# Kernel optimization log

Measured on AMD Instinct MI355X. Metric: run time of the kernel, lower is better.

## Reference

```python
import jax, jax.numpy as jnp
import numpy as np

B, NQ, NK = 2, 1024, 1024
QD, KVD, OD = 1024, 1024, 1024
H, DH = 8, 64
INNER = H * DH  # 512
FF_INNER = 4 * OD


def _ln(x, w, b, eps=1e-5):
    m = jnp.mean(x, axis=-1, keepdims=True)
    v = jnp.mean((x - m) ** 2, axis=-1, keepdims=True)
    return (x - m) / jnp.sqrt(v + eps) * w + b


def _attn(q, k, v, h):
    # q:[b,nq,h*d] k,v:[b,nk,h*d] -> [b,nq,h*d]
    b, nq, _ = q.shape
    nk = k.shape[1]
    qh = q.reshape(b, nq, h, -1).transpose(0, 2, 1, 3)
    kh = k.reshape(b, nk, h, -1).transpose(0, 2, 1, 3)
    vh = v.reshape(b, nk, h, -1).transpose(0, 2, 1, 3)
    scale = qh.shape[-1] ** -0.5
    sim = jnp.einsum('bhid,bhjd->bhij', qh * scale, kh)
    a = jax.nn.softmax(sim, axis=-1)
    o = jnp.einsum('bhij,bhjd->bhid', a, vh)
    return o.transpose(0, 2, 1, 3).reshape(b, nq, -1)


def setup_inputs() -> dict:
    key = jax.random.key(0)
    ks = jax.random.split(key, 16)
    w = lambda k, shp: jax.random.normal(k, shp, dtype=jnp.float32) * 0.02
    return {
        'query_feats': jax.random.normal(ks[0], (B, NQ, QD), dtype=jnp.float32),
        'kv_feats_wt': jax.random.normal(ks[1], (B, NK, KVD), dtype=jnp.float32),
        'nq_w': jnp.ones((QD,), jnp.float32), 'nq_b': jnp.zeros((QD,), jnp.float32),
        'nkv_w': jnp.ones((KVD,), jnp.float32), 'nkv_b': jnp.zeros((KVD,), jnp.float32),
        'wq_cross': w(ks[2], (INNER, QD)),
        'wkv_cross': w(ks[3], (2 * INNER, KVD)),
        'wqkv_self': w(ks[4], (3 * INNER, QD)),
        'gn_w': jnp.ones((INNER,), jnp.float32), 'gn_b': jnp.zeros((INNER,), jnp.float32),
        'mha_in_w': w(ks[5], (3 * INNER, INNER)),
        'mha_out_w': w(ks[6], (INNER, INNER)),
        'mix_w': w(ks[7], (2, INNER)), 'mix_b': jnp.zeros((2,), jnp.float32),
        'w_out': w(ks[8], (OD, INNER)),
        'ff_ln_w': jnp.ones((OD,), jnp.float32), 'ff_ln_b': jnp.zeros((OD,), jnp.float32),
        'ff_fc1': w(ks[9], (FF_INNER, OD)),
        'ff_fc2': w(ks[10], (OD, FF_INNER)),
        'ff_gate': jnp.ones((1,), jnp.float32),
    }


def reference(query_feats, kv_feats_wt, nq_w, nq_b, nkv_w, nkv_b, wq_cross,
              wkv_cross, wqkv_self, gn_w, gn_b, mha_in_w, mha_out_w, mix_w,
              mix_b, w_out, ff_ln_w, ff_ln_b, ff_fc1, ff_fc2, ff_gate):
    # mode == 'full'
    kvn = _ln(kv_feats_wt, nkv_w, nkv_b)

    # wt self-attention branch
    qkv_wt = kvn @ wqkv_self.T
    q_wt, k_wt, v_wt = jnp.split(qkv_wt, 3, axis=-1)
    wt_out = _attn(q_wt, k_wt, v_wt, H) @ w_out.T

    qn = _ln(query_feats, nq_w, nq_b)

    # cross attention
    q_c = qn @ wq_cross.T
    k_c, v_c = jnp.split(kvn @ wkv_cross.T, 2, axis=-1)
    cross_out = _attn(q_c, k_c, v_c, H)

    # self attention on query
    q_s, k_s, v_s = jnp.split(qn @ wqkv_self.T, 3, axis=-1)
    self_out = _attn(q_s, k_s, v_s, H)

    # gating MHA (shared gate_norm)
    son = _ln(self_out, gn_w, gn_b)
    con = _ln(cross_out, gn_w, gn_b)
    wq_g, wk_g, wv_g = jnp.split(mha_in_w, 3, axis=0)
    gate_ctx = _attn(son @ wq_g.T, con @ wk_g.T, con @ wv_g.T, H) @ mha_out_w.T

    mix = jax.nn.softmax(gate_ctx @ mix_w.T + mix_b, axis=-1)
    mixed = mix[..., 0:1] * self_out + mix[..., 1:2] * cross_out
    delta = mixed @ w_out.T

    # FeedForward with gate
    y = _ln(delta, ff_ln_w, ff_ln_b)
    y = jax.nn.gelu(y @ ff_fc1.T, approximate=False) @ ff_fc2.T
    delta = delta + ff_gate * y

    return jnp.stack([delta, wt_out])  # [2, B, NQ, OD]
```

## Files before the change

### kernel.cpp

```cpp
#include <hip/hip_runtime.h>
#include <math.h>


#define M_ROWS 2048
#define SEQ    1024

typedef unsigned short u16;
typedef __attribute__((ext_vector_type(8))) short short8;
typedef __attribute__((ext_vector_type(4))) float f32x4;

__device__ inline u16 f2b(float f) {
    unsigned u = __builtin_bit_cast(unsigned, f);
    u += 0x7FFFu + ((u >> 16) & 1u);
    return (u16)(u >> 16);
}
__device__ inline float b2f(u16 h) {
    return __builtin_bit_cast(float, (unsigned)h << 16);
}

__device__ inline void gload16(const u16* g, u16* l) {
    __builtin_amdgcn_global_load_lds(
        (const __attribute__((address_space(1))) void*)g,
        (__attribute__((address_space(3))) void*)l, 16, 0, 0);
}

__device__ __forceinline__ int aswz(int prow, int chunk) {
    return prow * 32 + ((chunk ^ ((prow >> 1) & 3)) << 3);
}

struct CvtPack { const float* s[8]; u16* d[8]; };

__global__ __launch_bounds__(256)
void cvt8_kernel(CvtPack p)
{
    constexpr int pre[9] = {0, 1536, 2048, 3072, 3840, 4096, 4608, 8704, 12800};
    const int b = blockIdx.x;
    int seg = 0;
    #pragma unroll
    for (int i = 1; i < 8; ++i) seg += (b >= pre[i]);
    const int off = (b - pre[seg]) * 1024 + threadIdx.x * 4;
    const float4 v = *reinterpret_cast<const float4*>(p.s[seg] + off);
    ushort4 o;
    o.x = f2b(v.x); o.y = f2b(v.y); o.z = f2b(v.z); o.w = f2b(v.w);
    *reinterpret_cast<ushort4*>(p.d[seg] + off) = o;
}

__global__ __launch_bounds__(256)
void ln_dual(const float* __restrict__ x0, const float* __restrict__ w0,
             const float* __restrict__ b0, u16* __restrict__ out0,
             const float* __restrict__ x1, const float* __restrict__ w1,
             const float* __restrict__ b1, u16* __restrict__ out1, int D)
{
    const int r = blockIdx.x;
    const int sel = r >= M_ROWS;
    const size_t row = sel ? r - M_ROWS : r;
    const float* x = sel ? x1 : x0;
    const float* w = sel ? w1 : w0;
    const float* bias = sel ? b1 : b0;
    u16* out = sel ? out1 : out0;
    const float* xr = x + row * (size_t)D;
    const int c = threadIdx.x * 4;
    float4 v = make_float4(0.f, 0.f, 0.f, 0.f);
    if (c < D) v = *reinterpret_cast<const float4*>(&xr[c]);
    float sum = v.x + v.y + v.z + v.w;
    float sq  = v.x*v.x + v.y*v.y + v.z*v.z + v.w*v.w;
    #pragma unroll
    for (int off = 32; off > 0; off >>= 1) {
        sum += __shfl_down(sum, off);
        sq  += __shfl_down(sq,  off);
    }
    __shared__ float s1[4], s2[4];
    const int wid = threadIdx.x >> 6;
    if ((threadIdx.x & 63) == 0) { s1[wid] = sum; s2[wid] = sq; }
    __syncthreads();
    const float tsum = s1[0] + s1[1] + s1[2] + s1[3];
    const float tsq  = s2[0] + s2[1] + s2[2] + s2[3];
    const float mean = tsum / (float)D;
    const float var  = tsq / (float)D - mean * mean;
    const float rstd = rsqrtf(var + 1e-5f);
    if (c < D) {
        ushort4 o;
        o.x = f2b((v.x - mean) * rstd * w[c+0] + bias[c+0]);
        o.y = f2b((v.y - mean) * rstd * w[c+1] + bias[c+1]);
        o.z = f2b((v.z - mean) * rstd * w[c+2] + bias[c+2]);
        o.w = f2b((v.w - mean) * rstd * w[c+3] + bias[c+3]);
        *reinterpret_cast<ushort4*>(&out[row * (size_t)D + c]) = o;
    }
}

__global__ __launch_bounds__(256)
void ln_bf16(const float* __restrict__ x, const float* __restrict__ w,
             const float* __restrict__ bias, u16* __restrict__ out, int D)
{
    const size_t row = blockIdx.x;
    const float* xr = x + row * (size_t)D;
    const int c = threadIdx.x * 4;
    float4 v = make_float4(0.f, 0.f, 0.f, 0.f);
    if (c < D) v = *reinterpret_cast<const float4*>(&xr[c]);
    float sum = v.x + v.y + v.z + v.w;
    float sq  = v.x*v.x + v.y*v.y + v.z*v.z + v.w*v.w;
    #pragma unroll
    for (int off = 32; off > 0; off >>= 1) {
        sum += __shfl_down(sum, off);
        sq  += __shfl_down(sq,  off);
    }
    __shared__ float s1[4], s2[4];
    const int wid = threadIdx.x >> 6;
    if ((threadIdx.x & 63) == 0) { s1[wid] = sum; s2[wid] = sq; }
    __syncthreads();
    const float tsum = s1[0] + s1[1] + s1[2] + s1[3];
    const float tsq  = s2[0] + s2[1] + s2[2] + s2[3];
    const float mean = tsum / (float)D;
    const float var  = tsq / (float)D - mean * mean;
    const float rstd = rsqrtf(var + 1e-5f);
    if (c < D) {
        ushort4 o;
        o.x = f2b((v.x - mean) * rstd * w[c+0] + bias[c+0]);
        o.y = f2b((v.y - mean) * rstd * w[c+1] + bias[c+1]);
        o.z = f2b((v.z - mean) * rstd * w[c+2] + bias[c+2]);
        o.w = f2b((v.w - mean) * rstd * w[c+3] + bias[c+3]);
        *reinterpret_cast<ushort4*>(&out[row * (size_t)D + c]) = o;
    }
}

__device__ __forceinline__ void gemm64_core(
    const u16* __restrict__ A, const u16* __restrict__ W, void* __restrict__ C,
    int ob, int N, int K, int m0, int n0, u16* As, u16* Ws)
{
    constexpr int PF = 3, LPT = 2, RD = 4;
    const int tid  = threadIdx.x;
    const int lane = tid & 63;
    const int wave = tid >> 6;
    const int wr = wave >> 1, wc = wave & 1;

    const int srow = tid >> 2;
    const int scol = (((tid & 3) ^ ((srow >> 1) & 3))) * 8;
    const u16* Ag = A + (size_t)(m0 + srow) * K + scol;
    const u16* Wg = W + (size_t)(n0 + srow) * K + scol;

    const int fr = lane & 15;
    const int fq = lane >> 4;

    f32x4 acc[2][2] = {};

    auto stage = [&](int buf, int k0) {
        gload16(Ag + k0, &As[buf * 2048 + tid * 8]);
        gload16(Wg + k0, &Ws[buf * 2048 + tid * 8]);
    };
    auto compute = [&](int buf) {
        short8 a[2], b[2];
        #pragma unroll
        for (int m = 0; m < 2; ++m) {
            const int r = wr * 32 + m * 16 + fr;
            a[m] = *reinterpret_cast<const short8*>(&As[buf * 2048 + aswz(r, fq)]);
        }
        #pragma unroll
        for (int n = 0; n < 2; ++n) {
            const int r = wc * 32 + n * 16 + fr;
            b[n] = *reinterpret_cast<const short8*>(&Ws[buf * 2048 + aswz(r, fq)]);
        }
        #pragma unroll
        for (int m = 0; m < 2; ++m)
            #pragma unroll
            for (int n = 0; n < 2; ++n)
                acc[m][n] = __builtin_amdgcn_mfma_f32_16x16x32_bf16(
                    a[m], b[n], acc[m][n], 0, 0, 0);
    };

    const int nt = K / 32;
    #pragma unroll
    for (int i = 0; i < PF; ++i) stage(i, i * 32);

    int cbuf = 0, sbuf = PF;
    for (int t = 0; t <= nt - PF; ++t) {
        asm volatile("s_waitcnt vmcnt(%0)\n\ts_barrier"
                     :: "n"((PF - 1) * LPT) : "memory");
        if (t + PF < nt) {
            stage(sbuf, (t + PF) * 32);
            if (++sbuf == RD) sbuf = 0;
        }
        compute(cbuf);
        if (++cbuf == RD) cbuf = 0;
    }
    #pragma unroll
    for (int i = 1; i < PF; ++i) {
        asm volatile("s_waitcnt vmcnt(%0)\n\ts_barrier"
                     :: "n"((PF - 1 - i) * LPT) : "memory");
        compute(cbuf);
        if (++cbuf == RD) cbuf = 0;
    }

    #pragma unroll
    for (int m = 0; m < 2; ++m)
        #pragma unroll
        for (int j = 0; j < 4; ++j) {
            const size_t row = (size_t)(m0 + wr * 32 + m * 16 + fq * 4 + j);
            #pragma unroll
            for (int n = 0; n < 2; ++n) {
                const size_t idx = row * (size_t)N + (size_t)(n0 + wc * 32 + n * 16 + fr);
                if (ob) ((u16*)C)[idx]  = f2b(acc[m][n][j]);
                else    ((float*)C)[idx] = acc[m][n][j];
            }
        }
}

__device__ __forceinline__ void gemm128_core(
    const u16* __restrict__ A, const u16* __restrict__ W, u16* __restrict__ C,
    int N, int K, int m0, int n0, u16* As, u16* Ws)
{
    constexpr int PF = 3, LPT = 3, RD = 4;
    const int tid  = threadIdx.x;
    const int lane = tid & 63;
    const int wave = tid >> 6;
    const int wr = wave >> 1, wc = wave & 1;

    const int srow = tid >> 2;
    const int scol = (((tid & 3) ^ ((srow >> 1) & 3))) * 8;
    const u16* Ag = A + (size_t)(m0 + srow) * K + scol;
    const u16* Wg = W + (size_t)(n0 + srow) * K + scol;

    const int fr = lane & 15;
    const int fq = lane >> 4;

    f32x4 acc[4][2] = {};

    auto stage = [&](int buf, int k0) {
        gload16(Ag + k0,                  &As[buf * 4096 + tid * 8]);
        gload16(Ag + k0 + (size_t)64 * K, &As[buf * 4096 + tid * 8 + 2048]);
        gload16(Wg + k0,                  &Ws[buf * 2048 + tid * 8]);
    };
    auto compute = [&](int buf) {
        short8 a[4], b[2];
        #pragma unroll
        for (int m = 0; m < 4; ++m) {
            const int r = wr * 64 + m * 16 + fr;
            a[m] = *reinterpret_cast<const short8*>(&As[buf * 4096 + aswz(r, fq)]);
        }
        #pragma unroll
        for (int n = 0; n < 2; ++n) {
            const int r = wc * 32 + n * 16 + fr;
            b[n] = *reinterpret_cast<const short8*>(&Ws[buf * 2048 + aswz(r, fq)]);
        }
        #pragma unroll
        for (int m = 0; m < 4; ++m)
            #pragma unroll
            for (int n = 0; n < 2; ++n)
                acc[m][n] = __builtin_amdgcn_mfma_f32_16x16x32_bf16(
                    a[m], b[n], acc[m][n], 0, 0, 0);
    };

    const int nt = K / 32;
    #pragma unroll
    for (int i = 0; i < PF; ++i) stage(i, i * 32);

    int cbuf = 0, sbuf = PF;
    for (int t = 0; t <= nt - PF; ++t) {
        asm volatile("s_waitcnt vmcnt(%0)\n\ts_barrier"
                     :: "n"((PF - 1) * LPT) : "memory");
        if (t + PF < nt) {
            stage(sbuf, (t + PF) * 32);
            if (++sbuf == RD) sbuf = 0;
        }
        compute(cbuf);
        if (++cbuf == RD) cbuf = 0;
    }
    #pragma unroll
    for (int i = 1; i < PF; ++i) {
        asm volatile("s_waitcnt vmcnt(%0)\n\ts_barrier"
                     :: "n"((PF - 1 - i) * LPT) : "memory");
        compute(cbuf);
        if (++cbuf == RD) cbuf = 0;
    }

    #pragma unroll
    for (int m = 0; m < 4; ++m)
        #pragma unroll
        for (int j = 0; j < 4; ++j) {
            const size_t row = (size_t)(m0 + wr * 64 + m * 16 + fq * 4 + j);
            #pragma unroll
            for (int n = 0; n < 2; ++n)
                C[row * (size_t)N + (size_t)(n0 + wc * 32 + n * 16 + fr)] =
                    f2b(acc[m][n][j]);
        }
}

template<int BM, int BN, int EPI, int OB>
__global__ __launch_bounds__(256)
void gemm_mfma(const u16* __restrict__ A, const u16* __restrict__ W,
               void* __restrict__ Cv, int N, int K,
               const float* __restrict__ gatep, int kchunk)
{
    constexpr int MF  = BM / 32;
    constexpr int NF  = BN / 32;
    constexpr int LPT = BM / 64 + BN / 64;
    constexpr int PF  = 3;
    constexpr int RD  = 4;
    __shared__ __align__(16) u16 As[RD][BM * 32];
    __shared__ __align__(16) u16 Ws[RD][BN * 32];
    const int tid  = threadIdx.x;
    const int lane = tid & 63;
    const int wave = tid >> 6;
    const int wr = wave >> 1, wc = wave & 1;

    const int nwg = gridDim.x * gridDim.y;
    const int bid = blockIdx.y * gridDim.x + blockIdx.x;
    const int nid = (bid & 7) * (nwg >> 3) + (bid >> 3);
    const int by  = nid % gridDim.y;
    const int bx  = nid / gridDim.y;
    const int m0 = by * BM, n0 = bx * BN;
    const int kz = blockIdx.z * kchunk;

    const int srow = tid >> 2;
    const int scol = (((tid & 3) ^ ((srow >> 1) & 3))) * 8;
    const u16* Ag = A + (size_t)(m0 + srow) * K + scol + kz;
    const u16* Wg = W + (size_t)(n0 + srow) * K + scol + kz;

    const int fr = lane & 15;
    const int fq = lane >> 4;

    f32x4 acc[MF][NF] = {};

    auto stage = [&](int buf, int k0) {
        #pragma unroll
        for (int i = 0; i < BM / 64; ++i)
            gload16(Ag + k0 + (size_t)(i * 64) * K, &As[buf][tid * 8 + i * 2048]);
        #pragma unroll
        for (int i = 0; i < BN / 64; ++i)
            gload16(Wg + k0 + (size_t)(i * 64) * K, &Ws[buf][tid * 8 + i * 2048]);
    };
    auto compute = [&](int buf) {
        short8 a[MF], b[NF];
        #pragma unroll
        for (int m = 0; m < MF; ++m) {
            const int r = wr * (BM / 2) + m * 16 + fr;
            a[m] = *reinterpret_cast<const short8*>(&As[buf][aswz(r, fq)]);
        }
        #pragma unroll
        for (int n = 0; n < NF; ++n) {
            const int r = wc * (BN / 2) + n * 16 + fr;
            b[n] = *reinterpret_cast<const short8*>(&Ws[buf][aswz(r, fq)]);
        }
        #pragma unroll
        for (int m = 0; m < MF; ++m)
            #pragma unroll
            for (int n = 0; n < NF; ++n)
                acc[m][n] = __builtin_amdgcn_mfma_f32_16x16x32_bf16(
                    a[m], b[n], acc[m][n], 0, 0, 0);
    };

    const int nt = kchunk / 32;
    #pragma unroll
    for (int i = 0; i < PF; ++i) stage(i, i * 32);

    int cbuf = 0, sbuf = PF;
    for (int t = 0; t <= nt - PF; ++t) {
        asm volatile("s_waitcnt vmcnt(%0)\n\ts_barrier"
                     :: "n"((PF - 1) * LPT) : "memory");
        if (t + PF < nt) {
            stage(sbuf, (t + PF) * 32);
            if (++sbuf == RD) sbuf = 0;
        }
        compute(cbuf);
        if (++cbuf == RD) cbuf = 0;
    }
    #pragma unroll
    for (int i = 1; i < PF; ++i) {
        asm volatile("s_waitcnt vmcnt(%0)\n\ts_barrier"
                     :: "n"((PF - 1 - i) * LPT) : "memory");
        compute(cbuf);
        if (++cbuf == RD) cbuf = 0;
    }

    float* Cz = (float*)Cv + (size_t)blockIdx.z * M_ROWS * N;
    const float gate = (EPI == 2) ? gatep[0] : 0.f;
    #pragma unroll
    for (int m = 0; m < MF; ++m) {
        #pragma unroll
        for (int j = 0; j < 4; ++j) {
            const size_t row = (size_t)(m0 + wr * (BM / 2) + m * 16 + fq * 4 + j);
            #pragma unroll
            for (int n = 0; n < NF; ++n) {
                float v = acc[m][n][j];
                const size_t idx = row * (size_t)N + (size_t)(n0 + wc * (BN / 2) + n * 16 + fr);
                if (EPI == 1) v = 0.5f * v * (1.f + erff(v * 0.70710678118654752f));
                if (OB) {
                    ((u16*)Cv)[idx] = f2b(v);
                } else {
                    if (EPI == 2) Cz[idx] = Cz[idx] + gate * v;
                    else          Cz[idx] = v;
                }
            }
        }
    }
}

struct GemmPack4 { const u16* A[4]; const u16* W[4]; u16* C[4]; int N[4]; };

__global__ __launch_bounds__(256)
void gemm_bat4(GemmPack4 p)
{
    __shared__ __align__(16) u16 As[4][4096];
    __shared__ __align__(16) u16 Ws[4][2048];
    constexpr int pre[5] = {0, 384, 512, 768, 1152};
    const int nwg = gridDim.x * gridDim.y;
    const int bid = blockIdx.y * gridDim.x + blockIdx.x;
    const int nid = (bid & 7) * (nwg >> 3) + (bid >> 3);
    int seg = 0;
    #pragma unroll
    for (int i = 1; i < 4; ++i) seg += (nid >= pre[i]);
    const int idx = nid - pre[seg];
    const int nx  = p.N[seg] >> 6;
    const int bx  = idx % nx;
    const int by  = idx / nx;
    gemm128_core(p.A[seg], p.W[seg], p.C[seg], p.N[seg], 1024,
                 by * 128, bx * 64, &As[0][0], &Ws[0][0]);
}

struct GemmPack4b { const u16* A[4]; const u16* W[4]; void* C[4]; int N[4]; int ob[4]; };

__global__ __launch_bounds__(256)
void gemm_bat4b(GemmPack4b p)
{
    __shared__ __align__(16) u16 As[4][2048];
    __shared__ __align__(16) u16 Ws[4][2048];
    constexpr int pre[5] = {0, 512, 768, 1024, 1280};
    const int nwg = gridDim.x * gridDim.y;
    const int bid = blockIdx.y * gridDim.x + blockIdx.x;
    const int nid = (bid & 7) * (nwg >> 3) + (bid >> 3);
    int seg = 0;
    #pragma unroll
    for (int i = 1; i < 4; ++i) seg += (nid >= pre[i]);
    const int idx = nid - pre[seg];
    const int nx  = p.N[seg] >> 6;
    const int bx  = idx % nx;
    const int by  = idx / nx;
    gemm64_core(p.A[seg], p.W[seg], p.C[seg], p.ob[seg], p.N[seg], 512,
                by * 64, bx * 64, &As[0][0], &Ws[0][0]);
}

__global__ __launch_bounds__(256)
void redk(const float* __restrict__ p, const float* __restrict__ gatep,
          float* __restrict__ C)
{
    const int i = (blockIdx.x * 256 + threadIdx.x) * 4;
    const float g = gatep[0];
    const float4 a = *reinterpret_cast<const float4*>(p + i);
    const float4 b = *reinterpret_cast<const float4*>(p + 2097152 + i);
    const float4 c = *reinterpret_cast<const float4*>(p + 4194304 + i);
    const float4 d = *reinterpret_cast<const float4*>(p + 6291456 + i);
    float4 o = *reinterpret_cast<float4*>(C + i);
    o.x += g * ((a.x + b.x) + (c.x + d.x));
    o.y += g * ((a.y + b.y) + (c.y + d.y));
    o.z += g * ((a.z + b.z) + (c.z + d.z));
    o.w += g * ((a.w + b.w) + (c.w + d.w));
    *reinterpret_cast<float4*>(C + i) = o;
}

struct AttnPack {
    const u16* Q[3]; const u16* K[3]; const u16* V[3]; void* O[3];
    int qs[3], ks[3], vs[3], os[3], ob[3];
};

__global__ __launch_bounds__(256)
void attn_mfma(AttnPack p, int NP)
{
    const int nwg = gridDim.x * gridDim.y;
    const int bid = blockIdx.y * gridDim.x + blockIdx.x;
    const int nid = (bid & 7) * (nwg >> 3) + (bid >> 3);
    const int z  = nid % NP;
    const int r_ = nid / NP;
    const int qt = r_ & 15;
    const int bh = r_ >> 4;

    const u16* __restrict__ Q = p.Q[z];
    const u16* __restrict__ K = p.K[z];
    const u16* __restrict__ V = p.V[z];
    void* __restrict__ Ov = p.O[z];
    const int qs = p.qs[z], ks = p.ks[z], vs = p.vs[z], os = p.os[z];
    const int ob = p.ob[z];

    __shared__ __align__(16) u16 Ks[2][128 * 32];
    __shared__ __align__(16) u16 Vt[2][128 * 32];
    __shared__ __align__(16) u16 Ps[4][32 * 32];
    const int tid  = threadIdx.x;
    const int lane = tid & 63;
    const int wave = tid >> 6;
    const int fr = lane & 15;
    const int fq = lane >> 4;

    const int b   = bh >> 3;
    const int hc  = (bh & 7) * 64;
    const size_t qrow0 = (size_t)b * SEQ + (size_t)qt * 64;
    const size_t krow0 = (size_t)b * SEQ;

    short8 qf[2];
    {
        const u16* qp = Q + (qrow0 + wave * 16 + fr) * qs + hc + fq * 8;
        qf[0] = *reinterpret_cast<const short8*>(qp);
        qf[1] = *reinterpret_cast<const short8*>(qp + 32);
    }

    const int skr = tid >> 2;
    const int skc = (tid & 3) * 16;
    const int svk = (tid >> 4) * 4;
    const int svd = (tid & 15) * 4;

    const int kprow = (skc >= 32 ? 64 : 0) + skr;
    const int kc0   = (skc & 31) >> 3;
    const int vbase  = (svk >= 32) ? 64 : 0;
    const int vchunk = (svk & 31) >> 3;
    const int vpos   = svk & 7;

    short8 kreg0, kreg1;
    ushort4 vr0, vr1, vr2, vr3;
    auto load_tile = [&](int kt) {
        const u16* kp = K + (krow0 + kt * 64 + skr) * ks + hc + skc;
        kreg0 = *reinterpret_cast<const short8*>(kp);
        kreg1 = *reinterpret_cast<const short8*>(kp + 8);
        const u16* vp = V + (krow0 + kt * 64 + svk) * vs + hc + svd;
        vr0 = *reinterpret_cast<const ushort4*>(vp);
        vr1 = *reinterpret_cast<const ushort4*>(vp + vs);
        vr2 = *reinterpret_cast<const ushort4*>(vp + 2 * (size_t)vs);
        vr3 = *reinterpret_cast<const ushort4*>(vp + 3 * (size_t)vs);
    };
    auto write_tile = [&](int bf) {
        *reinterpret_cast<short8*>(&Ks[bf][aswz(kprow, kc0)])     = kreg0;
        *reinterpret_cast<short8*>(&Ks[bf][aswz(kprow, kc0 + 1)]) = kreg1;
        uint2 w;
        #pragma unroll
        for (int i = 0; i < 4; ++i) {
            u16* dst = &Vt[bf][aswz(vbase + svd + i, vchunk) + vpos];
            unsigned lo, hi;
            if (i == 0) { lo = (unsigned)vr0.x | ((unsigned)vr1.x << 16);
                          hi = (unsigned)vr2.x | ((unsigned)vr3.x << 16); }
            else if (i == 1) { lo = (unsigned)vr0.y | ((unsigned)vr1.y << 16);
                               hi = (unsigned)vr2.y | ((unsigned)vr3.y << 16); }
            else if (i == 2) { lo = (unsigned)vr0.z | ((unsigned)vr1.z << 16);
                               hi = (unsigned)vr2.z | ((unsigned)vr3.z << 16); }
            else { lo = (unsigned)vr0.w | ((unsigned)vr1.w << 16);
                   hi = (unsigned)vr2.w | ((unsigned)vr3.w << 16); }
            w.x = lo; w.y = hi;
            *reinterpret_cast<uint2*>(dst) = w;
        }
    };

    float m_run = -1e30f, l_run = 0.f;
    f32x4 acc[4] = {};

    load_tile(0);
    write_tile(0);
    __syncthreads();

    constexpr int NT = SEQ / 64;
    for (int kt = 0; kt < NT; ++kt) {
        const int bf = kt & 1;
        if (kt + 1 < NT) load_tile(kt + 1);

        f32x4 st[4] = {};
        #pragma unroll
        for (int kn = 0; kn < 4; ++kn) {
            const int r = kn * 16 + fr;
            const short8 ka0 = *reinterpret_cast<const short8*>(
                &Ks[bf][aswz(r, fq)]);
            const short8 ka1 = *reinterpret_cast<const short8*>(
                &Ks[bf][aswz(64 + r, fq)]);
            st[kn] = __builtin_amdgcn_mfma_f32_16x16x32_bf16(ka0, qf[0], st[kn], 0, 0, 0);
            st[kn] = __builtin_amdgcn_mfma_f32_16x16x32_bf16(ka1, qf[1], st[kn], 0, 0, 0);
        }

        float mx = -1e30f;
        #pragma unroll
        for (int kn = 0; kn < 4; ++kn)
            #pragma unroll
            for (int r = 0; r < 4; ++r) {
                st[kn][r] *= 0.125f;
                mx = fmaxf(mx, st[kn][r]);
            }
        mx = fmaxf(mx, __shfl_xor(mx, 16, 64));
        mx = fmaxf(mx, __shfl_xor(mx, 32, 64));
        const float mnew = fmaxf(m_run, mx);
        const float corr = __expf(m_run - mnew);
        m_run = mnew;
        float psum = 0.f;
        #pragma unroll
        for (int kn = 0; kn < 4; ++kn) {
            const float p0 = __expf(st[kn][0] - mnew);
            const float p1 = __expf(st[kn][1] - mnew);
            const float p2 = __expf(st[kn][2] - mnew);
            const float p3 = __expf(st[kn][3] - mnew);
            psum += (p0 + p1) + (p2 + p3);
            uint2 w;
            w.x = (unsigned)f2b(p0) | ((unsigned)f2b(p1) << 16);
            w.y = (unsigned)f2b(p2) | ((unsigned)f2b(p3) << 16);
            const int prow = (kn >> 1) * 16 + fr;
            const int pcol = (kn & 1) * 16 + fq * 4;
            *reinterpret_cast<uint2*>(
                &Ps[wave][aswz(prow, pcol >> 3) + (pcol & 7)]) = w;
        }
        psum += __shfl_xor(psum, 16, 64);
        psum += __shfl_xor(psum, 32, 64);
        l_run = l_run * corr + psum;

        float cq[4];
        #pragma unroll
        for (int j = 0; j < 4; ++j) cq[j] = __shfl(corr, fq * 4 + j, 64);
        #pragma unroll
        for (int nd = 0; nd < 4; ++nd)
            #pragma unroll
            for (int j = 0; j < 4; ++j)
                acc[nd][j] *= cq[j];

        short8 pa0 = *reinterpret_cast<const short8*>(&Ps[wave][aswz(fr, fq)]);
        short8 pa1 = *reinterpret_cast<const short8*>(&Ps[wave][aswz(16 + fr, fq)]);
        #pragma unroll
        for (int nd = 0; nd < 4; ++nd) {
            const int d = nd * 16 + fr;
            const short8 vb0 = *reinterpret_cast<const short8*>(
                &Vt[bf][aswz(d, fq)]);
            const short8 vb1 = *reinterpret_cast<const short8*>(
                &Vt[bf][aswz(64 + d, fq)]);
            acc[nd] = __builtin_amdgcn_mfma_f32_16x16x32_bf16(pa0, vb0, acc[nd], 0, 0, 0);
            acc[nd] = __builtin_amdgcn_mfma_f32_16x16x32_bf16(pa1, vb1, acc[nd], 0, 0, 0);
        }

        if (kt + 1 < NT) write_tile(bf ^ 1);
        __syncthreads();
    }

    float iq[4];
    #pragma unroll
    for (int j = 0; j < 4; ++j) iq[j] = 1.f / __shfl(l_run, fq * 4 + j, 64);
    #pragma unroll
    for (int j = 0; j < 4; ++j) {
        const size_t orow = (qrow0 + wave * 16 + fq * 4 + j) * os + hc;
        #pragma unroll
        for (int nd = 0; nd < 4; ++nd) {
            const float v = acc[nd][j] * iq[j];
            if (ob) ((u16*)Ov)[orow + nd * 16 + fr] = f2b(v);
            else    ((float*)Ov)[orow + nd * 16 + fr] = v;
        }
    }
}

__global__ __launch_bounds__(256)
void mix_kernel(const float* __restrict__ gctx, const float* __restrict__ mixw,
                const float* __restrict__ mixb, const float* __restrict__ so,
                const float* __restrict__ co, u16* __restrict__ mixed)
{
    const size_t row = blockIdx.x;
    const float* g = gctx + row * 512;
    float d0 = 0.f, d1 = 0.f;
    for (int c = threadIdx.x; c < 512; c += 256) {
        const float gv = g[c];
        d0 = fmaf(gv, mixw[c], d0);
        d1 = fmaf(gv, mixw[512 + c], d1);
    }
    #pragma unroll
    for (int off = 32; off > 0; off >>= 1) {
        d0 += __shfl_down(d0, off);
        d1 += __shfl_down(d1, off);
    }
    __shared__ float sA[4], sB[4];
    const int wid = threadIdx.x >> 6;
    if ((threadIdx.x & 63) == 0) { sA[wid] = d0; sB[wid] = d1; }
    __syncthreads();
    const float t0 = sA[0] + sA[1] + sA[2] + sA[3] + mixb[0];
    const float t1 = sB[0] + sB[1] + sB[2] + sB[3] + mixb[1];
    const float mx = fmaxf(t0, t1);
    const float e0 = __expf(t0 - mx), e1 = __expf(t1 - mx);
    const float inv = 1.f / (e0 + e1);
    const float w0 = e0 * inv, w1 = e1 * inv;
    for (int c = threadIdx.x; c < 512; c += 256)
        mixed[row * 512 + c] = f2b(w0 * so[row * 512 + c] + w1 * co[row * 512 + c]);
}

extern "C" void kernel_launch(void* const* d_in, const int* in_sizes, int n_in,
                              void* d_out, int out_size, void* d_ws, size_t ws_size,
                              hipStream_t stream)
{
    const float* query     = (const float*)d_in[0];
    const float* kvwt      = (const float*)d_in[1];
    const float* nq_w      = (const float*)d_in[2];
    const float* nq_b      = (const float*)d_in[3];
    const float* nkv_w     = (const float*)d_in[4];
    const float* nkv_b     = (const float*)d_in[5];
    const float* wq_cross  = (const float*)d_in[6];
    const float* wkv_cross = (const float*)d_in[7];
    const float* wqkv_self = (const float*)d_in[8];
    const float* gn_w      = (const float*)d_in[9];
    const float* gn_b      = (const float*)d_in[10];
    const float* mha_in_w  = (const float*)d_in[11];
    const float* mha_out_w = (const float*)d_in[12];
    const float* mix_w     = (const float*)d_in[13];
    const float* mix_b     = (const float*)d_in[14];
    const float* w_out     = (const float*)d_in[15];
    const float* ff_ln_w   = (const float*)d_in[16];
    const float* ff_ln_b   = (const float*)d_in[17];
    const float* ff_fc1    = (const float*)d_in[18];
    const float* ff_fc2    = (const float*)d_in[19];
    const float* ff_gate   = (const float*)d_in[20];

    float* delta_out = (float*)d_out;
    float* wt_out    = (float*)d_out + (size_t)M_ROWS * 1024;

    char* wsb = (char*)d_ws;
    u16*   qkv_b   = (u16*)  (wsb + 0);
    u16*   kv_c_b  = (u16*)  (wsb + 6291456);
    u16*   q_c_b   = (u16*)  (wsb + 10485760);
    float* cross_f = (float*)(wsb + 12582912);
    float* self_f  = (float*)(wsb + 16777216);
    u16*   kvn_b   = (u16*)  (wsb + 20971520);
    u16*   qn_b    = (u16*)  (wsb + 25165824);
    u16*   wta_b   = (u16*)  (wsb + 29360128);
    u16*   con_b   = (u16*)  (wsb + 31457280);
    u16*   gq_b    = qkv_b;
    u16*   gk_b    = qkv_b + 1048576;
    u16*   gv_b    = qkv_b + 2097152;
    float* gctx_f  = (float*)kv_c_b;
    u16*   gattn_b = kvn_b;
    u16*   mixed_b = kvn_b + 1048576;
    u16*   lnd_b   = qn_b;
    u16*   ffh_b   = qkv_b;
    float* part_f  = (float*)(wsb + 16777216);
    u16*   qkv_s_b = (u16*)  (wsb + 59768832);
    u16*   son_b   = (u16*)  (wsb + 66060288);
    u16* wqkv_self_b = (u16*)(wsb + 33554432);
    u16* wq_cross_b  = (u16*)(wsb + 36700160);
    u16* wkv_cross_b = (u16*)(wsb + 37748736);
    u16* mha_in_b    = (u16*)(wsb + 39845888);
    u16* mha_out_b   = (u16*)(wsb + 41418752);
    u16* w_out_b     = (u16*)(wsb + 41943040);
    u16* ff_fc1_b    = (u16*)(wsb + 42991616);
    u16* ff_fc2_b    = (u16*)(wsb + 51380224);

    const dim3 blk(256);

    CvtPack cp;
    cp.s[0] = wqkv_self; cp.d[0] = wqkv_self_b;
    cp.s[1] = wq_cross;  cp.d[1] = wq_cross_b;
    cp.s[2] = wkv_cross; cp.d[2] = wkv_cross_b;
    cp.s[3] = mha_in_w;  cp.d[3] = mha_in_b;
    cp.s[4] = mha_out_w; cp.d[4] = mha_out_b;
    cp.s[5] = w_out;     cp.d[5] = w_out_b;
    cp.s[6] = ff_fc1;    cp.d[6] = ff_fc1_b;
    cp.s[7] = ff_fc2;    cp.d[7] = ff_fc2_b;
    cvt8_kernel<<<dim3(12800), blk, 0, stream>>>(cp);

    ln_dual<<<dim3(2 * M_ROWS), blk, 0, stream>>>(
        kvwt, nkv_w, nkv_b, kvn_b, query, nq_w, nq_b, qn_b, 1024);

    GemmPack4 g4;
    g4.A[0] = kvn_b; g4.W[0] = wqkv_self_b; g4.C[0] = qkv_b;   g4.N[0] = 1536;
    g4.A[1] = qn_b;  g4.W[1] = wq_cross_b;  g4.C[1] = q_c_b;   g4.N[1] = 512;
    g4.A[2] = kvn_b; g4.W[2] = wkv_cross_b; g4.C[2] = kv_c_b;  g4.N[2] = 1024;
    g4.A[3] = qn_b;  g4.W[3] = wqkv_self_b; g4.C[3] = qkv_s_b; g4.N[3] = 1536;
    gemm_bat4<<<dim3(36, 32), blk, 0, stream>>>(g4);

    AttnPack ap;
    ap.Q[0] = qkv_b;    ap.K[0] = qkv_b + 512;    ap.V[0] = qkv_b + 1024;    ap.O[0] = wta_b;
    ap.qs[0] = 1536; ap.ks[0] = 1536; ap.vs[0] = 1536; ap.os[0] = 512; ap.ob[0] = 1;
    ap.Q[1] = q_c_b;    ap.K[1] = kv_c_b;         ap.V[1] = kv_c_b + 512;    ap.O[1] = cross_f;
    ap.qs[1] = 512;  ap.ks[1] = 1024; ap.vs[1] = 1024; ap.os[1] = 512; ap.ob[1] = 0;
    ap.Q[2] = qkv_s_b;  ap.K[2] = qkv_s_b + 512;  ap.V[2] = qkv_s_b + 1024;  ap.O[2] = self_f;
    ap.qs[2] = 1536; ap.ks[2] = 1536; ap.vs[2] = 1536; ap.os[2] = 512; ap.ob[2] = 0;
    attn_mfma<<<dim3(48, 16), blk, 0, stream>>>(ap, 3);

    ln_dual<<<dim3(2 * M_ROWS), blk, 0, stream>>>(
        self_f, gn_w, gn_b, son_b, cross_f, gn_w, gn_b, con_b, 512);

    GemmPack4b g4b;
    g4b.A[0] = wta_b; g4b.W[0] = w_out_b;             g4b.C[0] = wt_out; g4b.N[0] = 1024; g4b.ob[0] = 0;
    g4b.A[1] = son_b; g4b.W[1] = mha_in_b;            g4b.C[1] = gq_b;   g4b.N[1] = 512;  g4b.ob[1] = 1;
    g4b.A[2] = con_b; g4b.W[2] = mha_in_b + 512*512;  g4b.C[2] = gk_b;   g4b.N[2] = 512;  g4b.ob[2] = 1;
    g4b.A[3] = con_b; g4b.W[3] = mha_in_b + 1024*512; g4b.C[3] = gv_b;   g4b.N[3] = 512;  g4b.ob[3] = 1;
    gemm_bat4b<<<dim3(40, 32), blk, 0, stream>>>(g4b);

    AttnPack gp;
    gp.Q[0] = gq_b; gp.K[0] = gk_b; gp.V[0] = gv_b; gp.O[0] = gattn_b;
    gp.qs[0] = 512; gp.ks[0] = 512; gp.vs[0] = 512; gp.os[0] = 512; gp.ob[0] = 1;
    gp.Q[1] = gp.Q[0]; gp.K[1] = gp.K[0]; gp.V[1] = gp.V[0]; gp.O[1] = gp.O[0];
    gp.qs[1] = 512; gp.ks[1] = 512; gp.vs[1] = 512; gp.os[1] = 512; gp.ob[1] = 1;
    gp.Q[2] = gp.Q[0]; gp.K[2] = gp.K[0]; gp.V[2] = gp.V[0]; gp.O[2] = gp.O[0];
    gp.qs[2] = 512; gp.ks[2] = 512; gp.vs[2] = 512; gp.os[2] = 512; gp.ob[2] = 1;
    attn_mfma<<<dim3(16, 16), blk, 0, stream>>>(gp, 1);
    gemm_mfma<64,64,0,0><<<dim3(8, 32), blk, 0, stream>>>(gattn_b, mha_out_b, gctx_f, 512, 512, nullptr, 512);
    mix_kernel<<<dim3(M_ROWS), blk, 0, stream>>>(gctx_f, mix_w, mix_b, self_f, cross_f, mixed_b);
    gemm_mfma<64,64,0,0><<<dim3(16, 32), blk, 0, stream>>>(mixed_b, w_out_b, delta_out, 1024, 512, nullptr, 512);
    ln_bf16<<<dim3(M_ROWS), blk, 0, stream>>>(delta_out, ff_ln_w, ff_ln_b, lnd_b, 1024);
    gemm_mfma<128,64,1,1><<<dim3(64, 16), blk, 0, stream>>>(lnd_b, ff_fc1_b, ffh_b, 4096, 1024, nullptr, 1024);
    gemm_mfma<128,64,0,0><<<dim3(16, 16, 4), blk, 0, stream>>>(ffh_b, ff_fc2_b, part_f, 1024, 4096, nullptr, 1024);
    redk<<<dim3(2048), blk, 0, stream>>>(part_f, ff_gate, delta_out);
}
```

Measured before the change: 262.6 us.

## Use 8-wave 128x128 GEMM tiles for batched projections and FFN GEMMs

Replaces the 4-wave 128x64 GEMM core with an 8-wave (512-thread) 128x128 tile core that cuts pipeline depth to 2 stages and 3 LDS buffers. It is used for the batched QKV projection and both feed-forward GEMMs, with GELU, fp32/bf16 output and split-K support folded into the core. Larger tiles raise operand reuse per block and halve the grid. The cost is fewer blocks per GPU and a shallower prefetch, which may expose memory latency.

```diff
diff --git a/kernel.cpp b/kernel.cpp
--- a/kernel.cpp
+++ b/kernel.cpp
@@ -204,20 +204,21 @@
         }
 }
 
-__device__ __forceinline__ void gemm128_core(
-    const u16* __restrict__ A, const u16* __restrict__ W, u16* __restrict__ C,
-    int N, int K, int m0, int n0, u16* As, u16* Ws)
-{
-    constexpr int PF = 3, LPT = 3, RD = 4;
+__device__ __forceinline__ void gemm8_core(
+    const u16* __restrict__ A, const u16* __restrict__ W, void* __restrict__ C,
+    int ob, int epi, int N, int Kstride, int kcnt, int m0, int n0,
+    u16* As, u16* Ws)
+{
+    constexpr int PF = 2, LPT = 2, RD = 3;
     const int tid  = threadIdx.x;
     const int lane = tid & 63;
     const int wave = tid >> 6;
-    const int wr = wave >> 1, wc = wave & 1;
+    const int wr = wave >> 2, wc = wave & 3;
 
     const int srow = tid >> 2;
     const int scol = (((tid & 3) ^ ((srow >> 1) & 3))) * 8;
-    const u16* Ag = A + (size_t)(m0 + srow) * K + scol;
-    const u16* Wg = W + (size_t)(n0 + srow) * K + scol;
+    const u16* Ag = A + (size_t)(m0 + srow) * Kstride + scol;
+    const u16* Wg = W + (size_t)(n0 + srow) * Kstride + scol;
 
     const int fr = lane & 15;
     const int fq = lane >> 4;
@@ -225,9 +226,8 @@
     f32x4 acc[4][2] = {};
 
     auto stage = [&](int buf, int k0) {
-        gload16(Ag + k0,                  &As[buf * 4096 + tid * 8]);
-        gload16(Ag + k0 + (size_t)64 * K, &As[buf * 4096 + tid * 8 + 2048]);
-        gload16(Wg + k0,                  &Ws[buf * 2048 + tid * 8]);
+        gload16(Ag + k0, &As[buf * 4096 + tid * 8]);
+        gload16(Wg + k0, &Ws[buf * 4096 + tid * 8]);
     };
     auto compute = [&](int buf) {
         short8 a[4], b[2];
@@ -239,7 +239,7 @@
         #pragma unroll
         for (int n = 0; n < 2; ++n) {
             const int r = wc * 32 + n * 16 + fr;
-            b[n] = *reinterpret_cast<const short8*>(&Ws[buf * 2048 + aswz(r, fq)]);
+            b[n] = *reinterpret_cast<const short8*>(&Ws[buf * 4096 + aswz(r, fq)]);
         }
         #pragma unroll
         for (int m = 0; m < 4; ++m)
@@ -249,7 +249,7 @@
                     a[m], b[n], acc[m][n], 0, 0, 0);
     };
 
-    const int nt = K / 32;
+    const int nt = kcnt / 32;
     #pragma unroll
     for (int i = 0; i < PF; ++i) stage(i, i * 32);
 
@@ -264,13 +264,8 @@
         compute(cbuf);
         if (++cbuf == RD) cbuf = 0;
     }
-    #pragma unroll
-    for (int i = 1; i < PF; ++i) {
-        asm volatile("s_waitcnt vmcnt(%0)\n\ts_barrier"
-                     :: "n"((PF - 1 - i) * LPT) : "memory");
-        compute(cbuf);
-        if (++cbuf == RD) cbuf = 0;
-    }
+    asm volatile("s_waitcnt vmcnt(0)\n\ts_barrier" ::: "memory");
+    compute(cbuf);
 
     #pragma unroll
     for (int m = 0; m < 4; ++m)
@@ -278,10 +273,53 @@
         for (int j = 0; j < 4; ++j) {
             const size_t row = (size_t)(m0 + wr * 64 + m * 16 + fq * 4 + j);
             #pragma unroll
-            for (int n = 0; n < 2; ++n)
-                C[row * (size_t)N + (size_t)(n0 + wc * 32 + n * 16 + fr)] =
-                    f2b(acc[m][n][j]);
-        }
+            for (int n = 0; n < 2; ++n) {
+                float v = acc[m][n][j];
+                if (epi == 1) v = 0.5f * v * (1.f + erff(v * 0.70710678118654752f));
+                const size_t idx = row * (size_t)N + (size_t)(n0 + wc * 32 + n * 16 + fr);
+                if (ob) ((u16*)C)[idx]  = f2b(v);
+                else    ((float*)C)[idx] = v;
+            }
+        }
+}
+
+__global__ __launch_bounds__(512)
+void gemm8(const u16* __restrict__ A, const u16* __restrict__ W,
+           void* __restrict__ Cv, int N, int K, int ob, int epi, int kchunk)
+{
+    __shared__ __align__(16) u16 As[3][4096];
+    __shared__ __align__(16) u16 Ws[3][4096];
+    const int nwg = gridDim.x * gridDim.y;
+    const int bid = blockIdx.y * gridDim.x + blockIdx.x;
+    const int nid = (bid & 7) * (nwg >> 3) + (bid >> 3);
+    const int by  = nid % gridDim.y;
+    const int bx  = nid / gridDim.y;
+    const int kz  = blockIdx.z * kchunk;
+    void* C = ob ? Cv : (void*)((float*)Cv + (size_t)blockIdx.z * M_ROWS * N);
+    gemm8_core(A + kz, W + kz, C, ob, epi, N, K, kchunk,
+               by * 128, bx * 128, &As[0][0], &Ws[0][0]);
+}
+
+struct GemmPack4 { const u16* A[4]; const u16* W[4]; u16* C[4]; int N[4]; };
+
+__global__ __launch_bounds__(512)
+void gemm8_bat4(GemmPack4 p)
+{
+    __shared__ __align__(16) u16 As[3][4096];
+    __shared__ __align__(16) u16 Ws[3][4096];
+    constexpr int pre[5] = {0, 192, 256, 384, 576};
+    const int nwg = gridDim.x * gridDim.y;
+    const int bid = blockIdx.y * gridDim.x + blockIdx.x;
+    const int nid = (bid & 7) * (nwg >> 3) + (bid >> 3);
+    int seg = 0;
+    #pragma unroll
+    for (int i = 1; i < 4; ++i) seg += (nid >= pre[i]);
+    const int idx = nid - pre[seg];
+    const int nx  = p.N[seg] >> 7;
+    const int bx  = idx % nx;
+    const int by  = idx / nx;
+    gemm8_core(p.A[seg], p.W[seg], p.C[seg], 1, 0, p.N[seg], 1024, 1024,
+               by * 128, bx * 128, &As[0][0], &Ws[0][0]);
 }
 
 template<int BM, int BN, int EPI, int OB>
@@ -392,28 +430,6 @@
             }
         }
     }
-}
-
-struct GemmPack4 { const u16* A[4]; const u16* W[4]; u16* C[4]; int N[4]; };
-
-__global__ __launch_bounds__(256)
-void gemm_bat4(GemmPack4 p)
-{
-    __shared__ __align__(16) u16 As[4][4096];
-    __shared__ __align__(16) u16 Ws[4][2048];
-    constexpr int pre[5] = {0, 384, 512, 768, 1152};
-    const int nwg = gridDim.x * gridDim.y;
-    const int bid = blockIdx.y * gridDim.x + blockIdx.x;
-    const int nid = (bid & 7) * (nwg >> 3) + (bid >> 3);
-    int seg = 0;
-    #pragma unroll
-    for (int i = 1; i < 4; ++i) seg += (nid >= pre[i]);
-    const int idx = nid - pre[seg];
-    const int nx  = p.N[seg] >> 6;
-    const int bx  = idx % nx;
-    const int by  = idx / nx;
-    gemm128_core(p.A[seg], p.W[seg], p.C[seg], p.N[seg], 1024,
-                 by * 128, bx * 64, &As[0][0], &Ws[0][0]);
 }
 
 struct GemmPack4b { const u16* A[4]; const u16* W[4]; void* C[4]; int N[4]; int ob[4]; };
@@ -734,6 +750,7 @@
     u16* ff_fc2_b    = (u16*)(wsb + 51380224);
 
     const dim3 blk(256);
+    const dim3 blk8(512);
 
     CvtPack cp;
     cp.s[0] = wqkv_self; cp.d[0] = wqkv_self_b;
@@ -754,7 +771,7 @@
     g4.A[1] = qn_b;  g4.W[1] = wq_cross_b;  g4.C[1] = q_c_b;   g4.N[1] = 512;
     g4.A[2] = kvn_b; g4.W[2] = wkv_cross_b; g4.C[2] = kv_c_b;  g4.N[2] = 1024;
     g4.A[3] = qn_b;  g4.W[3] = wqkv_self_b; g4.C[3] = qkv_s_b; g4.N[3] = 1536;
-    gemm_bat4<<<dim3(36, 32), blk, 0, stream>>>(g4);
+    gemm8_bat4<<<dim3(18, 32), blk8, 0, stream>>>(g4);
 
     AttnPack ap;
     ap.Q[0] = qkv_b;    ap.K[0] = qkv_b + 512;    ap.V[0] = qkv_b + 1024;    ap.O[0] = wta_b;
@@ -787,7 +804,7 @@
     mix_kernel<<<dim3(M_ROWS), blk, 0, stream>>>(gctx_f, mix_w, mix_b, self_f, cross_f, mixed_b);
     gemm_mfma<64,64,0,0><<<dim3(16, 32), blk, 0, stream>>>(mixed_b, w_out_b, delta_out, 1024, 512, nullptr, 512);
     ln_bf16<<<dim3(M_ROWS), blk, 0, stream>>>(delta_out, ff_ln_w, ff_ln_b, lnd_b, 1024);
-    gemm_mfma<128,64,1,1><<<dim3(64, 16), blk, 0, stream>>>(lnd_b, ff_fc1_b, ffh_b, 4096, 1024, nullptr, 1024);
-    gemm_mfma<128,64,0,0><<<dim3(16, 16, 4), blk, 0, stream>>>(ffh_b, ff_fc2_b, part_f, 1024, 4096, nullptr, 1024);
+    gemm8<<<dim3(32, 16), blk8, 0, stream>>>(lnd_b, ff_fc1_b, ffh_b, 4096, 1024, 1, 1, 1024);
+    gemm8<<<dim3(8, 16, 4), blk8, 0, stream>>>(ffh_b, ff_fc2_b, part_f, 1024, 4096, 0, 0, 1024);
     redk<<<dim3(2048), blk, 0, stream>>>(part_f, ff_gate, delta_out);
 }
```

Result: faster. 227.0 us (-13.6%).
